# Performance work log

Hardware: AMD Instinct MI355X
Metric: run time of the kernel (lower is better)

## Reference

```python
import jax, jax.numpy as jnp
import numpy as np

T = 0.07  # softmax temperature from __init__
N_QUEUES = 4


def _l2norm(x, axis):
    return x / jnp.maximum(jnp.linalg.norm(x, axis=axis, keepdims=True), 1e-12)


def setup_inputs() -> dict:
    key = jax.random.key(0)
    k1, k2, k3, k4, k5, k6 = jax.random.split(key, 6)
    N, D_in, dim, K = 512, 2048, 128, 65536
    im_q = jax.random.normal(k1, (N, D_in), dtype=jnp.float32)
    im_k = jax.random.normal(k2, (N, D_in), dtype=jnp.float32)
    W_q = jax.random.normal(k3, (D_in, dim), dtype=jnp.float32) * (1.0 / np.sqrt(D_in))
    W_k = jax.random.normal(k4, (D_in, dim), dtype=jnp.float32) * (1.0 / np.sqrt(D_in))
    queues = jax.random.normal(k5, (N_QUEUES, dim, K), dtype=jnp.float32)
    queues = _l2norm(queues, axis=1)  # normalize along feature dim, as in __init__
    label = jax.random.randint(k6, (N,), 0, 4, dtype=jnp.int32)
    return {"im_q": im_q, "im_k": im_k, "W_q": W_q, "W_k": W_k,
            "queues": queues, "label": label}


def reference(im_q, im_k, W_q, W_k, queues, label):
    # encoder_q / encoder_k abstracted as linear projections
    q = _l2norm(im_q @ W_q, axis=1)                      # [N, C]
    k = _l2norm(im_k @ W_k, axis=1)                      # [N, C] (no_grad in original)
    l_pos = jnp.einsum('nc,nc->n', q, k)[:, None]        # [N, 1]
    # per-sample queue routing: queue index = (label - 1) % 4
    route = jnp.mod(label - 1, N_QUEUES)                 # [N]
    onehot = jax.nn.one_hot(route, N_QUEUES, dtype=q.dtype)  # [N, G]
    # l_neg[n, k] = sum_c q[n, c] * queues[route[n], c, k], as grouped matmul
    l_neg = jnp.einsum('ngc,gck->nk', q[:, None, :] * onehot[:, :, None], queues)  # [N, K]
    logits = jnp.concatenate([l_pos, l_neg], axis=1) / T  # [N, 1+K]
    labels = jnp.zeros(logits.shape[0], dtype=jnp.int32)
    return logits, labels
```

## Files before the change

### kernel.cpp

```cpp
#include <hip/hip_runtime.h>

typedef short short8 __attribute__((ext_vector_type(8)));
typedef float floatx4 __attribute__((ext_vector_type(4)));

__device__ __forceinline__ unsigned short f2bf(float f) {
  unsigned u = __float_as_uint(f);
  u += 0x7FFFu + ((u >> 16) & 1u);
  return (unsigned short)(u >> 16);
}

__global__ __launch_bounds__(512, 4) void proj_partial(
    const float* __restrict__ im_q, const float* __restrict__ im_k,
    const float* __restrict__ Wq, const float* __restrict__ Wk,
    float* __restrict__ part, int* __restrict__ cnt) {
  __shared__ float imS[16 * 260];
  const int t = threadIdx.x;
  if (blockIdx.x == 0 && blockIdx.y == 0 && blockIdx.z == 0 && t < 4) cnt[t] = 0;
  const int which = blockIdx.z;
  const float* __restrict__ im = which ? im_k : im_q;
  const float* __restrict__ W  = which ? Wk : Wq;
  const int d0 = blockIdx.x * 256;
  const int row0 = blockIdx.y * 16;
#pragma unroll
  for (int p = 0; p < 2; ++p) {
    const int idx = t + p * 512;
    const int r = idx >> 6;
    const int dd = (idx & 63) * 4;
    *(float4*)(imS + r * 260 + dd) =
        *(const float4*)(im + (size_t)(row0 + r) * 2048 + d0 + dd);
  }
  __syncthreads();
  const int c4 = (t & 31) * 4;
  const int r  = t >> 5;
  float acc0 = 0.f, acc1 = 0.f, acc2 = 0.f, acc3 = 0.f;
  const float* __restrict__ Wp = W + (size_t)d0 * 128 + c4;
#pragma unroll 8
  for (int d = 0; d < 256; ++d) {
    const float4 w = *(const float4*)(Wp + (size_t)d * 128);
    const float a = imS[r * 260 + d];
    acc0 += a * w.x; acc1 += a * w.y; acc2 += a * w.z; acc3 += a * w.w;
  }
  *(float4*)(part + ((size_t)(which * 8 + blockIdx.x) * 512 + row0 + r) * 128 + c4) =
      make_float4(acc0, acc1, acc2, acc3);
}

__global__ __launch_bounds__(128) void finalize(
    const float* __restrict__ part, const int* __restrict__ label,
    unsigned short* __restrict__ qbf, int* __restrict__ cnt,
    int* __restrict__ rows, float* __restrict__ out) {
  const int n = blockIdx.x, c = threadIdx.x;
  float qraw = 0.f, kraw = 0.f;
#pragma unroll
  for (int ch = 0; ch < 8; ++ch) {
    qraw += part[((size_t)ch * 512 + n) * 128 + c];
    kraw += part[((size_t)(8 + ch) * 512 + n) * 128 + c];
  }
  float sq = qraw * qraw, sk = kraw * kraw, dt = qraw * kraw;
#pragma unroll
  for (int off = 32; off > 0; off >>= 1) {
    sq += __shfl_down(sq, off, 64);
    sk += __shfl_down(sk, off, 64);
    dt += __shfl_down(dt, off, 64);
  }
  __shared__ float sh[3][2];
  const int lane = c & 63, wv = c >> 6;
  if (lane == 0) { sh[0][wv] = sq; sh[1][wv] = sk; sh[2][wv] = dt; }
  __syncthreads();
  const float tsq = sh[0][0] + sh[0][1];
  const float tsk = sh[1][0] + sh[1][1];
  const float tdt = sh[2][0] + sh[2][1];
  const float nq = fmaxf(sqrtf(tsq), 1e-12f);
  const float nk = fmaxf(sqrtf(tsk), 1e-12f);
  qbf[n * 128 + c] = f2bf(qraw / nq);
  if (c == 0) {
    out[(size_t)n * 65537] = tdt / (nq * nk) * (1.0f / 0.07f);
    ((int*)out)[(size_t)512 * 65537 + n] = 0;
    int g = ((label[n] - 1) % 4 + 4) % 4;
    int pos = atomicAdd(cnt + g, 1);
    rows[g * 512 + pos] = n;
  }
}

__global__ __launch_bounds__(256) void qpack(
    const unsigned short* __restrict__ qbf, const int* __restrict__ cnt,
    const int* __restrict__ rows, unsigned short* __restrict__ Apack) {
  const int g = blockIdx.x >> 2, ch = blockIdx.x & 3;
  const int Mg = cnt[g];
  const int t = threadIdx.x;
#pragma unroll
  for (int w = 0; w < 8; ++w) {
    const int slot = w * 256 + t;
    const int kk = slot >> 9;
    const int rb = (slot >> 6) & 7;
    const int lane = slot & 63;
    const int l16 = lane & 15, qd = lane >> 4;
    const int m = ch * 128 + rb * 16 + l16;
    uint4 v = make_uint4(0u, 0u, 0u, 0u);
    if (m < Mg) {
      const int n = rows[g * 512 + m];
      v = *(const uint4*)(qbf + (size_t)n * 128 + kk * 32 + qd * 8);
    }
    *(uint4*)(Apack + ((size_t)blockIdx.x * 2048 + slot) * 8) = v;
  }
}

__global__ __launch_bounds__(256, 4) void moco_lneg(
    const float* __restrict__ queues, const unsigned short* __restrict__ Apack,
    const int* __restrict__ cnt, const int* __restrict__ rows,
    float* __restrict__ out) {
  __shared__ __align__(16) unsigned short Bs[128 * 136];
  __shared__ int rowsS[512];
  const int g = blockIdx.y;
  const int Mg = cnt[g];
  if (Mg == 0) return;
  const int t = threadIdx.x;
  const int j0 = blockIdx.x * 128;
  {
    const int j = t & 127;
    const int cb = (t >> 7) * 64;
    const float* __restrict__ qb = queues + (size_t)g * 128 * 65536 + j0 + j;
#pragma unroll 8
    for (int p = 0; p < 32; ++p) {
      const int c = cb + p * 2;
      const float f0 = qb[(size_t)c * 65536];
      const float f1 = qb[(size_t)(c + 1) * 65536];
      const unsigned u = (unsigned)f2bf(f0) | ((unsigned)f2bf(f1) << 16);
      *(unsigned*)(Bs + j * 136 + c) = u;
    }
  }
  for (int i = t; i < 512; i += 256) rowsS[i] = rows[g * 512 + i];
  __syncthreads();
  const int lane = t & 63, wave = t >> 6;
  const int qd = lane >> 4, l16 = lane & 15;
  const float invT = 1.0f / 0.07f;
  const int nch = (Mg + 127) >> 7;
  const unsigned short* __restrict__ Ag = Apack + (size_t)g * 4 * 16384 + lane * 8;
  for (int ch = 0; ch < nch; ++ch) {
    const int valid = min(Mg - ch * 128, 128);
    const unsigned short* __restrict__ Ab = Ag + (size_t)ch * 16384;
    floatx4 acc[8][2];
#pragma unroll
    for (int rb = 0; rb < 8; ++rb) {
      floatx4 z = {0.f, 0.f, 0.f, 0.f};
      acc[rb][0] = z; acc[rb][1] = z;
    }
    __builtin_amdgcn_s_setprio(1);
#pragma unroll
    for (int kk = 0; kk < 4; ++kk) {
      const int k0 = kk * 32 + qd * 8;
      const short8 bfrag0 = *(const short8*)&Bs[((wave * 2 + 0) * 16 + l16) * 136 + k0];
      const short8 bfrag1 = *(const short8*)&Bs[((wave * 2 + 1) * 16 + l16) * 136 + k0];
#pragma unroll
      for (int rb = 0; rb < 8; ++rb) {
        if (rb * 16 < valid) {
          const short8 afrag = *(const short8*)(Ab + kk * 4096 + rb * 512);
          acc[rb][0] = __builtin_amdgcn_mfma_f32_16x16x32_bf16(afrag, bfrag0, acc[rb][0], 0, 0, 0);
          acc[rb][1] = __builtin_amdgcn_mfma_f32_16x16x32_bf16(afrag, bfrag1, acc[rb][1], 0, 0, 0);
        }
      }
    }
    __builtin_amdgcn_s_setprio(0);
#pragma unroll
    for (int rb = 0; rb < 8; ++rb) {
      if (rb * 16 < valid) {
#pragma unroll
        for (int r = 0; r < 4; ++r) {
          const int ml = rb * 16 + qd * 4 + r;
          if (ml < valid) {
            const size_t base = (size_t)rowsS[ch * 128 + ml] * 65537 + 1 + j0;
            out[base + (wave * 2 + 0) * 16 + l16] = acc[rb][0][r] * invT;
            out[base + (wave * 2 + 1) * 16 + l16] = acc[rb][1][r] * invT;
          }
        }
      }
    }
  }
}

extern "C" void kernel_launch(void* const* d_in, const int* in_sizes, int n_in,
                              void* d_out, int out_size, void* d_ws, size_t ws_size,
                              hipStream_t stream) {
  const float* im_q   = (const float*)d_in[0];
  const float* im_k   = (const float*)d_in[1];
  const float* Wq     = (const float*)d_in[2];
  const float* Wk     = (const float*)d_in[3];
  const float* queues = (const float*)d_in[4];
  const int*   label  = (const int*)d_in[5];
  float* out = (float*)d_out;

  char* ws = (char*)d_ws;
  float* part = (float*)ws;
  unsigned short* qbf = (unsigned short*)(ws + (4u << 20));
  int* cnt  = (int*)(ws + (4u << 20) + (128u << 10));
  int* rows = cnt + 4;
  unsigned short* Apack = (unsigned short*)ws;

  proj_partial<<<dim3(8, 32, 2), 512, 0, stream>>>(im_q, im_k, Wq, Wk, part, cnt);
  finalize<<<512, 128, 0, stream>>>(part, label, qbf, cnt, rows, out);
  qpack<<<16, 256, 0, stream>>>(qbf, cnt, rows, Apack);
  moco_lneg<<<dim3(512, 4), 256, 0, stream>>>(queues, Apack, cnt, rows, out);
}
```

Before: 322.8 us.

## Load queue B fragments straight into registers and gather A rows in-kernel

Removes the qpack kernel and the LDS staging buffer for the queue tile. Each lane now reads its bf16 B fragments directly from global memory into registers, and gathers A fragments from qbf by indirecting through the per-group row list. This saves one kernel launch, the Apack round trip and the LDS traffic, and should improve occupancy now that LDS use is small. In exchange, the global reads of the queues become strided 16-float segments rather than 128-wide coalesced rows, the A gathers are irregular, and register pressure rises (launch bounds lowered to 3).

```diff
diff --git a/kernel.cpp b/kernel.cpp
--- a/kernel.cpp
+++ b/kernel.cpp
@@ -81,63 +81,44 @@
   }
 }
 
-__global__ __launch_bounds__(256) void qpack(
-    const unsigned short* __restrict__ qbf, const int* __restrict__ cnt,
-    const int* __restrict__ rows, unsigned short* __restrict__ Apack) {
-  const int g = blockIdx.x >> 2, ch = blockIdx.x & 3;
-  const int Mg = cnt[g];
-  const int t = threadIdx.x;
-#pragma unroll
-  for (int w = 0; w < 8; ++w) {
-    const int slot = w * 256 + t;
-    const int kk = slot >> 9;
-    const int rb = (slot >> 6) & 7;
-    const int lane = slot & 63;
-    const int l16 = lane & 15, qd = lane >> 4;
-    const int m = ch * 128 + rb * 16 + l16;
-    uint4 v = make_uint4(0u, 0u, 0u, 0u);
-    if (m < Mg) {
-      const int n = rows[g * 512 + m];
-      v = *(const uint4*)(qbf + (size_t)n * 128 + kk * 32 + qd * 8);
-    }
-    *(uint4*)(Apack + ((size_t)blockIdx.x * 2048 + slot) * 8) = v;
-  }
-}
-
-__global__ __launch_bounds__(256, 4) void moco_lneg(
-    const float* __restrict__ queues, const unsigned short* __restrict__ Apack,
+__global__ __launch_bounds__(256, 3) void moco_lneg(
+    const float* __restrict__ queues, const unsigned short* __restrict__ qbf,
     const int* __restrict__ cnt, const int* __restrict__ rows,
     float* __restrict__ out) {
-  __shared__ __align__(16) unsigned short Bs[128 * 136];
   __shared__ int rowsS[512];
   const int g = blockIdx.y;
   const int Mg = cnt[g];
   if (Mg == 0) return;
   const int t = threadIdx.x;
+  for (int i = t; i < 512; i += 256) rowsS[i] = rows[g * 512 + i];
+  const int lane = t & 63, wave = t >> 6;
+  const int qd = lane >> 4, l16 = lane & 15;
   const int j0 = blockIdx.x * 128;
+  short8 bf[4][2];
   {
-    const int j = t & 127;
-    const int cb = (t >> 7) * 64;
-    const float* __restrict__ qb = queues + (size_t)g * 128 * 65536 + j0 + j;
-#pragma unroll 8
-    for (int p = 0; p < 32; ++p) {
-      const int c = cb + p * 2;
-      const float f0 = qb[(size_t)c * 65536];
-      const float f1 = qb[(size_t)(c + 1) * 65536];
-      const unsigned u = (unsigned)f2bf(f0) | ((unsigned)f2bf(f1) << 16);
-      *(unsigned*)(Bs + j * 136 + c) = u;
+    const float* __restrict__ qb =
+        queues + ((size_t)(g * 128 + qd * 8)) * 65536 + j0 + l16;
+#pragma unroll
+    for (int kk = 0; kk < 4; ++kk) {
+#pragma unroll
+      for (int s = 0; s < 2; ++s) {
+        const float* __restrict__ p =
+            qb + (size_t)(kk * 32) * 65536 + (wave * 2 + s) * 16;
+        float f[8];
+#pragma unroll
+        for (int e = 0; e < 8; ++e) f[e] = p[(size_t)e * 65536];
+        unsigned* d = (unsigned*)&bf[kk][s];
+#pragma unroll
+        for (int i = 0; i < 4; ++i)
+          d[i] = (unsigned)f2bf(f[2 * i]) | ((unsigned)f2bf(f[2 * i + 1]) << 16);
+      }
     }
   }
-  for (int i = t; i < 512; i += 256) rowsS[i] = rows[g * 512 + i];
   __syncthreads();
-  const int lane = t & 63, wave = t >> 6;
-  const int qd = lane >> 4, l16 = lane & 15;
   const float invT = 1.0f / 0.07f;
   const int nch = (Mg + 127) >> 7;
-  const unsigned short* __restrict__ Ag = Apack + (size_t)g * 4 * 16384 + lane * 8;
   for (int ch = 0; ch < nch; ++ch) {
     const int valid = min(Mg - ch * 128, 128);
-    const unsigned short* __restrict__ Ab = Ag + (size_t)ch * 16384;
     floatx4 acc[8][2];
 #pragma unroll
     for (int rb = 0; rb < 8; ++rb) {
@@ -146,16 +127,16 @@
     }
     __builtin_amdgcn_s_setprio(1);
 #pragma unroll
-    for (int kk = 0; kk < 4; ++kk) {
-      const int k0 = kk * 32 + qd * 8;
-      const short8 bfrag0 = *(const short8*)&Bs[((wave * 2 + 0) * 16 + l16) * 136 + k0];
-      const short8 bfrag1 = *(const short8*)&Bs[((wave * 2 + 1) * 16 + l16) * 136 + k0];
+    for (int rb = 0; rb < 8; ++rb) {
+      if (rb * 16 < valid) {
+        const int m = rb * 16 + l16;
+        const int n = (m < valid) ? rowsS[ch * 128 + m] : 0;
+        const unsigned short* __restrict__ ap = qbf + (size_t)n * 128 + qd * 8;
 #pragma unroll
-      for (int rb = 0; rb < 8; ++rb) {
-        if (rb * 16 < valid) {
-          const short8 afrag = *(const short8*)(Ab + kk * 4096 + rb * 512);
-          acc[rb][0] = __builtin_amdgcn_mfma_f32_16x16x32_bf16(afrag, bfrag0, acc[rb][0], 0, 0, 0);
-          acc[rb][1] = __builtin_amdgcn_mfma_f32_16x16x32_bf16(afrag, bfrag1, acc[rb][1], 0, 0, 0);
+        for (int kk = 0; kk < 4; ++kk) {
+          const short8 afrag = *(const short8*)(ap + kk * 32);
+          acc[rb][0] = __builtin_amdgcn_mfma_f32_16x16x32_bf16(afrag, bf[kk][0], acc[rb][0], 0, 0, 0);
+          acc[rb][1] = __builtin_amdgcn_mfma_f32_16x16x32_bf16(afrag, bf[kk][1], acc[rb][1], 0, 0, 0);
         }
       }
     }
@@ -193,10 +174,8 @@
   unsigned short* qbf = (unsigned short*)(ws + (4u << 20));
   int* cnt  = (int*)(ws + (4u << 20) + (128u << 10));
   int* rows = cnt + 4;
-  unsigned short* Apack = (unsigned short*)ws;
 
   proj_partial<<<dim3(8, 32, 2), 512, 0, stream>>>(im_q, im_k, Wq, Wk, part, cnt);
   finalize<<<512, 128, 0, stream>>>(part, label, qbf, cnt, rows, out);
-  qpack<<<16, 256, 0, stream>>>(qbf, cnt, rows, Apack);
-  moco_lneg<<<dim3(512, 4), 256, 0, stream>>>(queues, Apack, cnt, rows, out);
+  moco_lneg<<<dim3(512, 4), 256, 0, stream>>>(queues, qbf, cnt, rows, out);
 }
```

After: 330.1 us. 1.02x slower.
